# Optimization experiments

Measured on AMD Instinct MI355X. Metric: run time of the kernel, lower is better.

Reference implementation:

```python
import jax, jax.numpy as jnp
import numpy as np
import math

H = 300
B = 2048
SEG = 48
N = B * SEG

def _gru_direction(x_seq, h0, w_ih, w_hh, b_ih, b_hh, reverse):
    # x_seq: [L, B, H]; h0: [B, H]; w_ih/w_hh: [3H, H]; b_ih/b_hh: [3H]
    xp = jnp.einsum('lbh,gh->lbg', x_seq, w_ih) + b_ih  # precompute input projections [L,B,3H]
    def step(h, xp_t):
        hp = h @ w_hh.T + b_hh
        xr, xz, xn = jnp.split(xp_t, 3, axis=-1)
        hr, hz, hn = jnp.split(hp, 3, axis=-1)
        r = jax.nn.sigmoid(xr + hr)
        z = jax.nn.sigmoid(xz + hz)
        n = jnp.tanh(xn + r * hn)
        h_new = (1.0 - z) * n + z * h
        return h_new, h_new
    _, ys = jax.lax.scan(step, h0, xp, reverse=reverse)
    return ys  # [L, B, H]

def setup_inputs() -> dict:
    key = jax.random.key(0)
    ks = jax.random.split(key, 12)
    bound = 1.0 / math.sqrt(H)
    u = lambda k, shape: jax.random.uniform(k, shape, jnp.float32, -bound, bound)
    x = jax.random.normal(ks[0], (N, H), jnp.float32)
    batch = jnp.repeat(jnp.arange(B, dtype=jnp.int32), SEG)  # sorted segment ids
    return {
        'x': x,
        'batch': batch,
        'num_moles': B,
        'max_len': SEG,
        'bias': u(ks[1], (H,)),
        'w_ih_f': u(ks[2], (3 * H, H)),
        'w_hh_f': u(ks[3], (3 * H, H)),
        'b_ih_f': u(ks[4], (3 * H,)),
        'b_hh_f': u(ks[5], (3 * H,)),
        'w_ih_b': u(ks[6], (3 * H, H)),
        'w_hh_b': u(ks[7], (3 * H, H)),
        'b_ih_b': u(ks[8], (3 * H,)),
        'b_hh_b': u(ks[9], (3 * H,)),
    }

def reference(x, batch, num_moles, max_len, bias, w_ih_f, w_hh_f, b_ih_f, b_hh_f, w_ih_b, w_hh_b, b_ih_b, b_hh_b):
    n, h = x.shape
    message = jax.nn.relu(x + bias)
    counts = jax.ops.segment_sum(jnp.ones_like(batch), batch, num_segments=num_moles)
    offsets = jnp.cumsum(counts) - counts
    pos = jnp.arange(n, dtype=batch.dtype) - offsets[batch]  # position within molecule
    # ragged -> padded pack [B, L, H]
    padded = jnp.zeros((num_moles, max_len, h), x.dtype).at[batch, pos].set(message)
    # initial hidden = per-molecule max over raw x (same h0 for both directions)
    h0 = jax.ops.segment_max(x, batch, num_segments=num_moles)  # [B, H]
    xs = padded.transpose(1, 0, 2)  # [L, B, H]
    yf = _gru_direction(xs, h0, w_ih_f, w_hh_f, b_ih_f, b_hh_f, reverse=False)
    yb = _gru_direction(xs, h0, w_ih_b, w_hh_b, b_ih_b, b_hh_b, reverse=True)
    y = jnp.concatenate([yf, yb], axis=-1).transpose(1, 0, 2)  # [B, L, 2H]
    return y[batch, pos]  # unpad -> [N, 2H]
```

## Files before the change

kernel.cpp:

```cpp
#include <hip/hip_runtime.h>
#include <hip/hip_bf16.h>

#define H    300
#define KP   320
#define BM   2048
#define SEG  48
#define NTOK (BM*SEG)
#define G    900
#define GP   912
#define NT   57
#define GW   1024
#define XPW  912
#define MOLW 16
#define WGT  1024
#define NPAIR (MOLW*150)
#define PIT  3

typedef __attribute__((ext_vector_type(8))) short short8;
typedef __attribute__((ext_vector_type(4))) float f32x4;

__device__ __forceinline__ float lo16(unsigned u) { return __uint_as_float(u << 16); }
__device__ __forceinline__ float hi16(unsigned u) { return __uint_as_float(u & 0xffff0000u); }
__device__ __forceinline__ unsigned short bfb(float f) {
    __hip_bfloat16 b = __float2bfloat16(f);
    return *(unsigned short*)&b;
}

__global__ void prep_weights(const float* wih_f, const float* whh_f, const float* bih_f,
                             const float* wih_b, const float* whh_b, const float* bih_b,
                             __hip_bfloat16* wih, __hip_bfloat16* whh, float* bih) {
    int idx = blockIdx.x * 256 + threadIdx.x;
    const int wih_n = 2 * GW * KP;
    const int whh_n = 2 * GP * KP;
    if (idx < wih_n) {
        int d = idx / (GW * KP);
        int r = (idx / KP) % GW;
        int k = idx % KP;
        const float* src = d ? wih_b : wih_f;
        float v = (r < G && k < H) ? src[r * H + k] : 0.f;
        wih[idx] = __float2bfloat16(v);
        return;
    }
    idx -= wih_n;
    if (idx < whh_n) {
        int d = idx / (GP * KP);
        int r = (idx / KP) % GP;
        int k = idx % KP;
        const float* src = d ? whh_b : whh_f;
        float v = (r < G && k < H) ? src[r * H + k] : 0.f;
        whh[idx] = __float2bfloat16(v);
        return;
    }
    idx -= whh_n;
    if (idx < 2 * GW) {
        int d = idx / GW;
        int r = idx % GW;
        const float* src = d ? bih_b : bih_f;
        bih[idx] = (r < G) ? src[r] : 0.f;
    }
}

__global__ void prep_msg(const float* x, const float* bias, __hip_bfloat16* msg) {
    int idx = blockIdx.x * 256 + threadIdx.x;
    if (idx >= NTOK * KP) return;
    int i = idx / KP, k = idx % KP;
    float v = 0.f;
    if (k < H) {
        v = x[i * H + k] + bias[k];
        v = v > 0.f ? v : 0.f;
    }
    msg[idx] = __float2bfloat16(v);
}

__global__ void h0_kernel(const float* x, float* h0) {
    int m = blockIdx.x;
    for (int c = threadIdx.x; c < H; c += blockDim.x) {
        const float* base = x + (long long)m * SEG * H + c;
        float v = -INFINITY;
        for (int t = 0; t < SEG; t++) v = fmaxf(v, base[t * H]);
        h0[m * H + c] = v;
    }
}

__global__ __launch_bounds__(256) void xp_gemm(const __hip_bfloat16* msg, const __hip_bfloat16* wih,
                                               const float* bih, __hip_bfloat16* xp) {
    int d = blockIdx.z;
    const short* A  = (const short*)msg;
    const short* Bw = (const short*)(wih + d * GW * KP);
    const float* bi = bih + d * GW;
    __hip_bfloat16* out = xp + (long long)d * NTOK * XPW;

    int lane = threadIdx.x & 63;
    int wid  = threadIdx.x >> 6;
    int l15  = lane & 15, quad = lane >> 4;
    int mbase = blockIdx.x * 128 + (wid >> 1) * 64;
    int nbase = blockIdx.y * 128 + (wid & 1) * 64;

    f32x4 acc[4][4] = {};
    for (int kc = 0; kc < KP; kc += 32) {
        int koff = kc + quad * 8;
        short8 a[4], b[4];
#pragma unroll
        for (int i = 0; i < 4; i++)
            a[i] = *(const short8*)(A + (mbase + i * 16 + l15) * KP + koff);
#pragma unroll
        for (int j = 0; j < 4; j++)
            b[j] = *(const short8*)(Bw + (nbase + j * 16 + l15) * KP + koff);
#pragma unroll
        for (int i = 0; i < 4; i++)
#pragma unroll
            for (int j = 0; j < 4; j++)
                acc[i][j] = __builtin_amdgcn_mfma_f32_16x16x32_bf16(a[i], b[j], acc[i][j], 0, 0, 0);
    }
#pragma unroll
    for (int i = 0; i < 4; i++)
#pragma unroll
        for (int j = 0; j < 4; j++) {
            int col = nbase + j * 16 + l15;
            float bv = bi[col];
            if (col < XPW) {
#pragma unroll
                for (int r = 0; r < 4; r++) {
                    int row = mbase + i * 16 + quad * 4 + r;
                    out[(long long)row * XPW + col] = __float2bfloat16(acc[i][j][r] + bv);
                }
            }
        }
}

__global__ __launch_bounds__(WGT, 4) void gru_kernel(const __hip_bfloat16* whh_all, const float* bhh_f,
                                                     const float* bhh_b, const __hip_bfloat16* xp,
                                                     const float* h0, float* out) {
    int grp = blockIdx.x;
    int d   = blockIdx.y;
    const short* Ws = (const short*)(whh_all + d * GP * KP);
    const float* bhh = d ? bhh_b : bhh_f;
    const __hip_bfloat16* xpd = xp + (long long)d * NTOK * XPW;

    int tid = threadIdx.x;
    int lane = tid & 63, wid = tid >> 6;
    int l15 = lane & 15, quad = lane >> 4;

    __shared__ __hip_bfloat16 hB[MOLW * 328];
    __shared__ __hip_bfloat16 hp[MOLW * GP];
    const short* hBs = (const short*)hB;

    int mol0 = grp * MOLW;

    for (int e = tid; e < MOLW * 328; e += WGT) hB[e] = __float2bfloat16(0.f);

    float bvw[4];
#pragma unroll
    for (int k = 0; k < 4; k++) {
        int nt = wid + 16 * k;
        int gc = nt * 16 + l15;
        bvw[k] = (nt < NT && gc < G) ? bhh[gc] : 0.f;
    }
    __syncthreads();

    float hv0[PIT], hv1[PIT];
#pragma unroll
    for (int i = 0; i < PIT; i++) {
        int e2 = tid + i * WGT;
        if (e2 < NPAIR) {
            int m = e2 / 150, c = 2 * (e2 % 150);
            float2 hh = *(const float2*)(h0 + (size_t)(mol0 + m) * H + c);
            hv0[i] = hh.x; hv1[i] = hh.y;
            unsigned pack = ((unsigned)bfb(hh.y) << 16) | bfb(hh.x);
            *(unsigned*)(&hB[m * 328 + c]) = pack;
        }
    }
    __syncthreads();

    for (int t = 0; t < SEG; t++) {
        int tt = d ? (SEG - 1 - t) : t;

        unsigned pr[PIT], pz[PIT], pn[PIT];
#pragma unroll
        for (int i = 0; i < PIT; i++) {
            int e2 = tid + i * WGT;
            if (e2 < NPAIR) {
                int m = e2 / 150, c = 2 * (e2 % 150);
                const __hip_bfloat16* xrow = xpd + ((long long)(mol0 + m) * SEG + tt) * XPW;
                pr[i] = *(const unsigned*)(xrow + c);
                pz[i] = *(const unsigned*)(xrow + c + 300);
                pn[i] = *(const unsigned*)(xrow + c + 600);
            }
        }

        short8 afA[10];
#pragma unroll
        for (int kk = 0; kk < 10; kk++) {
            int koff = kk * 32 + quad * 8;
            afA[kk] = *(const short8*)(hBs + l15 * 328 + koff);
        }

        int k8 = 0;
        for (int nt = wid; nt < NT; nt += 16, k8++) {
            int gcol = nt * 16 + l15;
            const short* bp = Ws + gcol * KP;
            f32x4 acc0 = {0.f, 0.f, 0.f, 0.f};
#pragma unroll
            for (int kk = 0; kk < 10; kk++) {
                short8 b = *(const short8*)(bp + kk * 32 + quad * 8);
                acc0 = __builtin_amdgcn_mfma_f32_16x16x32_bf16(afA[kk], b, acc0, 0, 0, 0);
            }
            float bv = bvw[k8];
#pragma unroll
            for (int r = 0; r < 4; r++)
                hp[(quad * 4 + r) * GP + gcol] = __float2bfloat16(acc0[r] + bv);
        }
        __syncthreads();

#pragma unroll
        for (int i = 0; i < PIT; i++) {
            int e2 = tid + i * WGT;
            if (e2 < NPAIR) {
                int m = e2 / 150, c = 2 * (e2 % 150);
                unsigned hr2 = *(const unsigned*)(&hp[m * GP + c]);
                unsigned hz2 = *(const unsigned*)(&hp[m * GP + c + 300]);
                unsigned hn2 = *(const unsigned*)(&hp[m * GP + c + 600]);

                float xr0 = lo16(pr[i]), xr1 = hi16(pr[i]);
                float xz0 = lo16(pz[i]), xz1 = hi16(pz[i]);
                float xn0 = lo16(pn[i]), xn1 = hi16(pn[i]);
                float hr0 = lo16(hr2),  hr1 = hi16(hr2);
                float hz0 = lo16(hz2),  hz1 = hi16(hz2);
                float hn0 = lo16(hn2),  hn1 = hi16(hn2);

                float rg0 = 1.f / (1.f + __expf(-(xr0 + hr0)));
                float rg1 = 1.f / (1.f + __expf(-(xr1 + hr1)));
                float zg0 = 1.f / (1.f + __expf(-(xz0 + hz0)));
                float zg1 = 1.f / (1.f + __expf(-(xz1 + hz1)));
                float ni0 = xn0 + rg0 * hn0;
                float ni1 = xn1 + rg1 * hn1;
                float ng0 = 1.f - 2.f / (__expf(2.f * ni0) + 1.f);
                float ng1 = 1.f - 2.f / (__expf(2.f * ni1) + 1.f);
                float h0n = (1.f - zg0) * ng0 + zg0 * hv0[i];
                float h1n = (1.f - zg1) * ng1 + zg1 * hv1[i];
                hv0[i] = h0n; hv1[i] = h1n;

                unsigned pack = ((unsigned)bfb(h1n) << 16) | bfb(h0n);
                *(unsigned*)(&hB[m * 328 + c]) = pack;

                long long tok = (long long)(mol0 + m) * SEG + tt;
                *(float2*)(out + tok * 600 + d * 300 + c) = make_float2(h0n, h1n);
            }
        }
        __syncthreads();
    }
}

extern "C" void kernel_launch(void* const* d_in, const int* in_sizes, int n_in,
                              void* d_out, int out_size, void* d_ws, size_t ws_size,
                              hipStream_t stream) {
    const float* x     = (const float*)d_in[0];
    const float* bias  = (const float*)d_in[4];
    const float* wih_f = (const float*)d_in[5];
    const float* whh_f = (const float*)d_in[6];
    const float* bih_f = (const float*)d_in[7];
    const float* bhh_f = (const float*)d_in[8];
    const float* wih_b = (const float*)d_in[9];
    const float* whh_b = (const float*)d_in[10];
    const float* bih_b = (const float*)d_in[11];
    const float* bhh_b = (const float*)d_in[12];
    float* out = (float*)d_out;

    char* ws = (char*)d_ws;
    __hip_bfloat16* msg = (__hip_bfloat16*)(ws);
    __hip_bfloat16* wih = (__hip_bfloat16*)(ws + 62914560LL);
    __hip_bfloat16* whh = (__hip_bfloat16*)(ws + 64225280LL);
    float*          bih = (float*)         (ws + 65392640LL);
    float*          h0  = (float*)         (ws + 65400832LL);
    __hip_bfloat16* xp  = (__hip_bfloat16*)(ws + 67858432LL);

    hipLaunchKernelGGL(prep_weights, dim3((2*GW*KP + 2*GP*KP + 2*GW + 255) / 256), dim3(256), 0, stream,
                       wih_f, whh_f, bih_f, wih_b, whh_b, bih_b, wih, whh, bih);
    hipLaunchKernelGGL(prep_msg, dim3((NTOK * KP + 255) / 256), dim3(256), 0, stream, x, bias, msg);
    hipLaunchKernelGGL(h0_kernel, dim3(BM), dim3(256), 0, stream, x, h0);
    hipLaunchKernelGGL(xp_gemm, dim3(NTOK / 128, GW / 128, 2), dim3(256), 0, stream, msg, wih, bih, xp);
    hipLaunchKernelGGL(gru_kernel, dim3(BM / MOLW, 2), dim3(WGT), 0, stream, whh, bhh_f, bhh_b, xp, h0, out);
}
```

Before: 1.733 ms.

## Stage xp GEMM tiles through LDS and software-pipeline GRU recurrent loads

New measurement: 1.610 ms. 1.08x faster.

```diff
diff --git a/kernel.cpp b/kernel.cpp
--- a/kernel.cpp
+++ b/kernel.cpp
@@ -15,6 +15,7 @@
 #define WGT  1024
 #define NPAIR (MOLW*150)
 #define PIT  3
+#define BKX  64
 
 typedef __attribute__((ext_vector_type(8))) short short8;
 typedef __attribute__((ext_vector_type(4))) float f32x4;
@@ -24,6 +25,10 @@
 __device__ __forceinline__ unsigned short bfb(float f) {
     __hip_bfloat16 b = __float2bfloat16(f);
     return *(unsigned short*)&b;
+}
+__device__ __forceinline__ void gload16(const void* g, void* l) {
+    __builtin_amdgcn_global_load_lds((const __attribute__((address_space(1))) unsigned*)g,
+                                     (__attribute__((address_space(3))) unsigned*)l, 16, 0, 0);
 }
 
 __global__ void prep_weights(const float* wih_f, const float* whh_f, const float* bih_f,
@@ -85,43 +90,69 @@
 __global__ __launch_bounds__(256) void xp_gemm(const __hip_bfloat16* msg, const __hip_bfloat16* wih,
                                                const float* bih, __hip_bfloat16* xp) {
     int d = blockIdx.z;
-    const short* A  = (const short*)msg;
-    const short* Bw = (const short*)(wih + d * GW * KP);
+    const __hip_bfloat16* A  = msg;
+    const __hip_bfloat16* Bw = wih + d * GW * KP;
     const float* bi = bih + d * GW;
     __hip_bfloat16* out = xp + (long long)d * NTOK * XPW;
 
-    int lane = threadIdx.x & 63;
-    int wid  = threadIdx.x >> 6;
-    int l15  = lane & 15, quad = lane >> 4;
-    int mbase = blockIdx.x * 128 + (wid >> 1) * 64;
-    int nbase = blockIdx.y * 128 + (wid & 1) * 64;
+    __shared__ __hip_bfloat16 sA[128 * BKX];
+    __shared__ __hip_bfloat16 sB[128 * BKX];
+    const short* sAs = (const short*)sA;
+    const short* sBs = (const short*)sB;
+
+    int tid = threadIdx.x;
+    int lane = tid & 63, wid = tid >> 6;
+    int l15 = lane & 15, quad = lane >> 4;
+    int mblk = blockIdx.x * 128, nblk = blockIdx.y * 128;
+    int mbase = (wid >> 1) * 64, nbase = (wid & 1) * 64;
+
+    int srow = wid * 32 + (lane >> 3);
+    int scc  = (lane & 7) ^ (srow & 7);
+    const short* gA0 = (const short*)A  + (long long)(mblk + srow) * KP + scc * 8;
+    const short* gB0 = (const short*)Bw + (long long)(nblk + srow) * KP + scc * 8;
+    int xsw = (l15 & 7) << 3;
 
     f32x4 acc[4][4] = {};
-    for (int kc = 0; kc < KP; kc += 32) {
-        int koff = kc + quad * 8;
-        short8 a[4], b[4];
+    for (int kc = 0; kc < KP / BKX; kc++) {
+#pragma unroll
+        for (int j = 0; j < 4; j++)
+            gload16(gA0 + (long long)j * 8 * KP + kc * BKX, (char*)sA + (wid * 4 + j) * 1024);
+#pragma unroll
+        for (int j = 0; j < 4; j++)
+            gload16(gB0 + (long long)j * 8 * KP + kc * BKX, (char*)sB + (wid * 4 + j) * 1024);
+        __syncthreads();
+
+        short8 af[4][2], bf[4][2];
 #pragma unroll
         for (int i = 0; i < 4; i++)
-            a[i] = *(const short8*)(A + (mbase + i * 16 + l15) * KP + koff);
+#pragma unroll
+            for (int kh = 0; kh < 2; kh++)
+                af[i][kh] = *(const short8*)(sAs + (mbase + i * 16 + l15) * BKX + ((kh * 32 + quad * 8) ^ xsw));
 #pragma unroll
         for (int j = 0; j < 4; j++)
-            b[j] = *(const short8*)(Bw + (nbase + j * 16 + l15) * KP + koff);
+#pragma unroll
+            for (int kh = 0; kh < 2; kh++)
+                bf[j][kh] = *(const short8*)(sBs + (nbase + j * 16 + l15) * BKX + ((kh * 32 + quad * 8) ^ xsw));
 #pragma unroll
         for (int i = 0; i < 4; i++)
 #pragma unroll
-            for (int j = 0; j < 4; j++)
-                acc[i][j] = __builtin_amdgcn_mfma_f32_16x16x32_bf16(a[i], b[j], acc[i][j], 0, 0, 0);
-    }
+            for (int j = 0; j < 4; j++) {
+                acc[i][j] = __builtin_amdgcn_mfma_f32_16x16x32_bf16(af[i][0], bf[j][0], acc[i][j], 0, 0, 0);
+                acc[i][j] = __builtin_amdgcn_mfma_f32_16x16x32_bf16(af[i][1], bf[j][1], acc[i][j], 0, 0, 0);
+            }
+        __syncthreads();
+    }
+
 #pragma unroll
     for (int i = 0; i < 4; i++)
 #pragma unroll
         for (int j = 0; j < 4; j++) {
-            int col = nbase + j * 16 + l15;
-            float bv = bi[col];
+            int col = nblk + nbase + j * 16 + l15;
             if (col < XPW) {
+                float bv = bi[col];
 #pragma unroll
                 for (int r = 0; r < 4; r++) {
-                    int row = mbase + i * 16 + quad * 4 + r;
+                    int row = mblk + mbase + i * 16 + quad * 4 + r;
                     out[(long long)row * XPW + col] = __float2bfloat16(acc[i][j][r] + bv);
                 }
             }
@@ -149,12 +180,24 @@
 
     for (int e = tid; e < MOLW * 328; e += WGT) hB[e] = __float2bfloat16(0.f);
 
+    const short* bpp[4];
     float bvw[4];
 #pragma unroll
     for (int k = 0; k < 4; k++) {
         int nt = wid + 16 * k;
+        int ntc = (nt < NT) ? nt : wid;
+        bpp[k] = Ws + (ntc * 16 + l15) * KP;
         int gc = nt * 16 + l15;
         bvw[k] = (nt < NT && gc < G) ? bhh[gc] : 0.f;
+    }
+
+    int m_[PIT], c_[PIT], xoff[PIT];
+#pragma unroll
+    for (int i = 0; i < PIT; i++) {
+        int e2 = tid + i * WGT;
+        int e2c = (e2 < NPAIR) ? e2 : 0;
+        m_[i] = e2c / 150; c_[i] = 2 * (e2c % 150);
+        xoff[i] = (mol0 + m_[i]) * SEG * XPW + c_[i];
     }
     __syncthreads();
 
@@ -163,67 +206,94 @@
     for (int i = 0; i < PIT; i++) {
         int e2 = tid + i * WGT;
         if (e2 < NPAIR) {
-            int m = e2 / 150, c = 2 * (e2 % 150);
-            float2 hh = *(const float2*)(h0 + (size_t)(mol0 + m) * H + c);
+            float2 hh = *(const float2*)(h0 + (size_t)(mol0 + m_[i]) * H + c_[i]);
             hv0[i] = hh.x; hv1[i] = hh.y;
             unsigned pack = ((unsigned)bfb(hh.y) << 16) | bfb(hh.x);
-            *(unsigned*)(&hB[m * 328 + c]) = pack;
+            *(unsigned*)(&hB[m_[i] * 328 + c_[i]]) = pack;
         }
     }
     __syncthreads();
+
+    unsigned pcr[PIT], pcz[PIT], pcn[PIT];
+    {
+        int tt0 = d ? (SEG - 1) : 0;
+#pragma unroll
+        for (int i = 0; i < PIT; i++) {
+            if (tid + i * WGT < NPAIR) {
+                const __hip_bfloat16* xr = xpd + xoff[i] + tt0 * XPW;
+                pcr[i] = *(const unsigned*)(xr);
+                pcz[i] = *(const unsigned*)(xr + 300);
+                pcn[i] = *(const unsigned*)(xr + 600);
+            }
+        }
+    }
 
     for (int t = 0; t < SEG; t++) {
         int tt = d ? (SEG - 1 - t) : t;
 
-        unsigned pr[PIT], pz[PIT], pn[PIT];
+        f32x4 acc[4] = {};
+        short8 bq[3][4];
+        short8 aq[2];
+#pragma unroll
+        for (int k = 0; k < 4; k++) {
+            bq[0][k] = *(const short8*)(bpp[k] + 0 * 32 + quad * 8);
+            bq[1][k] = *(const short8*)(bpp[k] + 1 * 32 + quad * 8);
+            bq[2][k] = *(const short8*)(bpp[k] + 2 * 32 + quad * 8);
+        }
+        aq[0] = *(const short8*)(hBs + l15 * 328 + 0 * 32 + quad * 8);
+        aq[1] = *(const short8*)(hBs + l15 * 328 + 1 * 32 + quad * 8);
+#pragma unroll
+        for (int kk = 0; kk < 10; kk++) {
+#pragma unroll
+            for (int k = 0; k < 4; k++)
+                acc[k] = __builtin_amdgcn_mfma_f32_16x16x32_bf16(aq[kk & 1], bq[kk % 3][k], acc[k], 0, 0, 0);
+            if (kk < 7) {
+#pragma unroll
+                for (int k = 0; k < 4; k++)
+                    bq[kk % 3][k] = *(const short8*)(bpp[k] + (kk + 3) * 32 + quad * 8);
+            }
+            if (kk < 8)
+                aq[kk & 1] = *(const short8*)(hBs + l15 * 328 + (kk + 2) * 32 + quad * 8);
+        }
+
+        unsigned pnr[PIT] = {0}, pnz[PIT] = {0}, pnn[PIT] = {0};
+        if (t + 1 < SEG) {
+            int tn = d ? (SEG - 2 - t) : (t + 1);
+#pragma unroll
+            for (int i = 0; i < PIT; i++) {
+                if (tid + i * WGT < NPAIR) {
+                    const __hip_bfloat16* xr = xpd + xoff[i] + tn * XPW;
+                    pnr[i] = *(const unsigned*)(xr);
+                    pnz[i] = *(const unsigned*)(xr + 300);
+                    pnn[i] = *(const unsigned*)(xr + 600);
+                }
+            }
+        }
+
+#pragma unroll
+        for (int k = 0; k < 4; k++) {
+            int nt = wid + 16 * k;
+            if (nt < NT) {
+                int gcol = nt * 16 + l15;
+#pragma unroll
+                for (int r = 0; r < 4; r++)
+                    hp[(quad * 4 + r) * GP + gcol] = __float2bfloat16(acc[k][r] + bvw[k]);
+            }
+        }
+        __syncthreads();
+
 #pragma unroll
         for (int i = 0; i < PIT; i++) {
             int e2 = tid + i * WGT;
             if (e2 < NPAIR) {
-                int m = e2 / 150, c = 2 * (e2 % 150);
-                const __hip_bfloat16* xrow = xpd + ((long long)(mol0 + m) * SEG + tt) * XPW;
-                pr[i] = *(const unsigned*)(xrow + c);
-                pz[i] = *(const unsigned*)(xrow + c + 300);
-                pn[i] = *(const unsigned*)(xrow + c + 600);
-            }
-        }
-
-        short8 afA[10];
-#pragma unroll
-        for (int kk = 0; kk < 10; kk++) {
-            int koff = kk * 32 + quad * 8;
-            afA[kk] = *(const short8*)(hBs + l15 * 328 + koff);
-        }
-
-        int k8 = 0;
-        for (int nt = wid; nt < NT; nt += 16, k8++) {
-            int gcol = nt * 16 + l15;
-            const short* bp = Ws + gcol * KP;
-            f32x4 acc0 = {0.f, 0.f, 0.f, 0.f};
-#pragma unroll
-            for (int kk = 0; kk < 10; kk++) {
-                short8 b = *(const short8*)(bp + kk * 32 + quad * 8);
-                acc0 = __builtin_amdgcn_mfma_f32_16x16x32_bf16(afA[kk], b, acc0, 0, 0, 0);
-            }
-            float bv = bvw[k8];
-#pragma unroll
-            for (int r = 0; r < 4; r++)
-                hp[(quad * 4 + r) * GP + gcol] = __float2bfloat16(acc0[r] + bv);
-        }
-        __syncthreads();
-
-#pragma unroll
-        for (int i = 0; i < PIT; i++) {
-            int e2 = tid + i * WGT;
-            if (e2 < NPAIR) {
-                int m = e2 / 150, c = 2 * (e2 % 150);
+                int m = m_[i], c = c_[i];
                 unsigned hr2 = *(const unsigned*)(&hp[m * GP + c]);
                 unsigned hz2 = *(const unsigned*)(&hp[m * GP + c + 300]);
                 unsigned hn2 = *(const unsigned*)(&hp[m * GP + c + 600]);
 
-                float xr0 = lo16(pr[i]), xr1 = hi16(pr[i]);
-                float xz0 = lo16(pz[i]), xz1 = hi16(pz[i]);
-                float xn0 = lo16(pn[i]), xn1 = hi16(pn[i]);
+                float xr0 = lo16(pcr[i]), xr1 = hi16(pcr[i]);
+                float xz0 = lo16(pcz[i]), xz1 = hi16(pcz[i]);
+                float xn0 = lo16(pcn[i]), xn1 = hi16(pcn[i]);
                 float hr0 = lo16(hr2),  hr1 = hi16(hr2);
                 float hz0 = lo16(hz2),  hz1 = hi16(hz2);
                 float hn0 = lo16(hn2),  hn1 = hi16(hn2);
@@ -247,6 +317,8 @@
                 *(float2*)(out + tok * 600 + d * 300 + c) = make_float2(h0n, h1n);
             }
         }
+#pragma unroll
+        for (int i = 0; i < PIT; i++) { pcr[i] = pnr[i]; pcz[i] = pnz[i]; pcn[i] = pnn[i]; }
         __syncthreads();
     }
 }
```
